# Performance work log

Hardware: AMD Instinct MI355X
Metric: run time of the kernel (lower is better)

The kernel has to match this reference:

```python
import jax, jax.numpy as jnp
import numpy as np

BETA_MAX = 0.995
BETA_MIN = 0.05
EPI_AGE_PENALTY = 0.02
EPI_STRENGTH_BOOST = 0.5
EPI_STRENGTH_DECAY = 0.995
EPI_WRITE_ALPHA = 0.5
EVICT_AGE_BOOST = 0.05
EVICT_STR_PENALTY = 0.5
SLOT_TEMP = 50.0
SWITCH_TAU = 0.5

B, H, K, U, OBS, SSUM, PROJ = 2048, 256, 32, 128, 128, 128, 128


def setup_inputs() -> dict:
    key = jax.random.key(0)
    ks = jax.random.split(key, 20)
    def gl(k, shape, fan_in):
        return jax.random.normal(k, shape, jnp.float32) / np.sqrt(fan_in).astype(np.float32)
    inp = {}
    inp['h_prev'] = jax.random.normal(ks[0], (B, H), jnp.float32)
    inp['keys'] = jax.random.normal(ks[1], (B, K, H), jnp.float32)
    inp['vals'] = jax.random.normal(ks[2], (B, K, H), jnp.float32)
    inp['age'] = jax.random.uniform(ks[3], (B, K), jnp.float32) * 100.0
    inp['strength'] = jax.random.uniform(ks[4], (B, K), jnp.float32)
    inp['obs'] = jax.random.normal(ks[5], (B, OBS), jnp.float32)
    inp['ssum'] = jax.random.normal(ks[6], (B, SSUM), jnp.float32)
    inp['u_int_prev'] = jax.random.normal(ks[7], (B, U), jnp.float32)
    inp['step_in_macro'] = jax.random.randint(ks[8], (B,), 0, 4, jnp.int32)
    # learned parameters
    inp['W_obs'] = gl(ks[9], (OBS, PROJ), OBS); inp['b_obs'] = jnp.zeros((PROJ,), jnp.float32)
    inp['W_ssum'] = gl(ks[10], (SSUM, PROJ), SSUM); inp['b_ssum'] = jnp.zeros((PROJ,), jnp.float32)
    XIN = 2 * PROJ
    inp['Wi'] = gl(ks[11], (XIN, 3 * H), XIN); inp['bi'] = jnp.zeros((3 * H,), jnp.float32)
    inp['Wh'] = gl(ks[12], (H, 3 * H), H); inp['bhn'] = jnp.zeros((H,), jnp.float32)
    inp['W_gate'] = gl(ks[13], (H, 1), H); inp['b_gate'] = jnp.zeros((1,), jnp.float32)
    inp['W_mean'] = gl(ks[14], (2 * H, U), 2 * H); inp['b_mean'] = jnp.zeros((U,), jnp.float32)
    inp['u_logstd'] = jnp.full((U,), -1.0, jnp.float32)
    inp['W_beta'] = gl(ks[15], (2 * H, 1), 2 * H); inp['b_beta'] = jnp.zeros((1,), jnp.float32)
    inp['W_sw'] = gl(ks[16], (2 * H, 1), 2 * H); inp['b_sw'] = jnp.zeros((1,), jnp.float32)
    return inp


def reference(h_prev, keys, vals, age, strength, obs, ssum, u_int_prev, step_in_macro,
              W_obs, b_obs, W_ssum, b_ssum, Wi, bi, Wh, bhn, W_gate, b_gate,
              W_mean, b_mean, u_logstd, W_beta, b_beta, W_sw, b_sw):
    Kslots = keys.shape[1]
    # input projections + GRU step (flax GRUCell: h' = (1-z)*n + z*h)
    xo = jnp.tanh(obs @ W_obs + b_obs)
    xs = jnp.tanh(ssum @ W_ssum + b_ssum)
    x_in = jnp.concatenate([xo, xs], axis=-1)
    gi = x_in @ Wi + bi
    gh = h_prev @ Wh
    ir, iz, inn = jnp.split(gi, 3, axis=-1)
    hr, hz, hn = jnp.split(gh, 3, axis=-1)
    r = jax.nn.sigmoid(ir + hr)
    z = jax.nn.sigmoid(iz + hz)
    n = jnp.tanh(inn + r * (hn + bhn))
    h_t = (1.0 - z) * n + z * h_prev
    # write gate
    w_str = jax.nn.sigmoid(h_t @ W_gate + b_gate)  # [B,1]
    # episodic slot memory: cosine-sim read
    qn = h_t / (jnp.linalg.norm(h_t, axis=-1, keepdims=True) + 1e-6)
    kn = keys / (jnp.linalg.norm(keys, axis=-1, keepdims=True) + 1e-6)
    sim_r = jnp.einsum('bkd,bd->bk', kn, qn)
    logits = sim_r + EPI_STRENGTH_BOOST * jnp.log(jnp.clip(strength, 1e-3, 1.0)) - EPI_AGE_PENALTY * age
    w_read = jax.nn.softmax(logits, axis=-1)
    read_out = jnp.einsum('bk,bkd->bd', w_read, vals)
    # write addressing (write_vec == query_vec == h_t so sim_w == sim_r)
    wk_n = qn
    sim_w = sim_r
    evict = EVICT_AGE_BOOST * jnp.log1p(age) - EVICT_STR_PENALTY * strength
    write_soft = jax.nn.softmax(sim_w * SLOT_TEMP + evict, axis=-1)
    write_hard = jax.nn.one_hot(jnp.argmax(write_soft, axis=-1), Kslots, dtype=jnp.float32)
    write_w = jax.lax.stop_gradient(write_hard - write_soft) + write_soft  # straight-through
    ws = jnp.clip(w_str, 0.0, 1.0)  # [B,1]
    eff_rate = write_w * ws * EPI_WRITE_ALPHA  # [B,K]
    rate = eff_rate[:, :, None]
    keys_new = (1.0 - rate) * keys + rate * wk_n[:, None, :]
    vals_new = (1.0 - rate) * vals + rate * h_t[:, None, :]
    age_new = (age + 1.0) * (1.0 - write_w)
    str_new = strength * EPI_STRENGTH_DECAY
    str_new = jnp.clip(str_new + write_w * ws * (1.0 - str_new), 0.0, 1.0)
    # heads
    ctx = jnp.concatenate([h_t, read_out], axis=-1)
    mean = ctx @ W_mean + b_mean
    beta = BETA_MIN + (BETA_MAX - BETA_MIN) * jax.nn.sigmoid((ctx @ W_beta + b_beta)[:, 0])
    sw_prob = jax.nn.sigmoid((ctx @ W_sw + b_sw)[:, 0])
    # deterministic path (rng=None): u_prop = mean, threshold switch
    u_prop = mean
    switch_f = jnp.where(sw_prob > SWITCH_TAU, 1.0, 0.0)
    is_boundary = jnp.where(step_in_macro == 0, 1.0, 0.0)
    switch_f = jnp.maximum(switch_f, is_boundary)
    sw_f = switch_f[:, None]
    beta_eff = beta[:, None] * (1.0 - sw_f)
    u_int = beta_eff * u_int_prev + (1.0 - beta_eff) * u_prop
    return (h_t, keys_new, vals_new, age_new, str_new, u_prop,
            switch_f.astype(jnp.int32), u_int, beta, sw_prob)
```

## Files before the change

kernel.cpp:

```cpp
#include <hip/hip_runtime.h>
#include <math.h>

#define Bdim 2048
#define Hdim 256
#define KS 32
#define Udim 128
#define OBSD 128
#define PROJD 128
#define H3 768

__device__ __forceinline__ float sigm(float x){ return 1.0f/(1.0f+__expf(-x)); }

typedef float __attribute__((ext_vector_type(4))) f32x4;

__device__ __forceinline__ float4 ntload4(const float* p){
    f32x4 v = __builtin_nontemporal_load((const f32x4*)p);
    return make_float4(v.x, v.y, v.z, v.w);
}
__device__ __forceinline__ void ntstore4(float* p, float4 q){
    f32x4 v = {q.x, q.y, q.z, q.w};
    __builtin_nontemporal_store(v, (f32x4*)p);
}

__global__ __launch_bounds__(256) void kA1(
    const float* __restrict__ obs, const float* __restrict__ ssum,
    const float* __restrict__ W_obs, const float* __restrict__ b_obs,
    const float* __restrict__ W_ssum, const float* __restrict__ b_ssum,
    float* __restrict__ xin)
{
    __shared__ float s_in[2][8][128];
    const int t = threadIdx.x;
    const int r0 = blockIdx.x * 8;

    {
        int r = t >> 5, c4 = (t & 31) << 2;
        float4 v = *(const float4*)(obs + (size_t)(r0+r)*OBSD + c4);
        s_in[0][r][c4+0]=v.x; s_in[0][r][c4+1]=v.y; s_in[0][r][c4+2]=v.z; s_in[0][r][c4+3]=v.w;
        v = *(const float4*)(ssum + (size_t)(r0+r)*OBSD + c4);
        s_in[1][r][c4+0]=v.x; s_in[1][r][c4+1]=v.y; s_in[1][r][c4+2]=v.z; s_in[1][r][c4+3]=v.w;
    }
    __syncthreads();

    const int col = t & 127;
    const int src = t >> 7;
    const float* Wp = src ? W_ssum : W_obs;
    const float bb = src ? b_ssum[col] : b_obs[col];

    float acc[8] = {0,0,0,0,0,0,0,0};
    for (int i=0;i<128;i++){
        float w = Wp[i*PROJD + col];
        #pragma unroll
        for (int r=0;r<8;r++) acc[r] = fmaf(s_in[src][r][i], w, acc[r]);
    }
    #pragma unroll
    for (int r=0;r<8;r++)
        xin[(size_t)(r0+r)*256 + t] = tanhf(acc[r] + bb);
}

__global__ __launch_bounds__(256) void kG2(
    const float* __restrict__ xin, const float* __restrict__ hp,
    const float* __restrict__ Wi, const float* __restrict__ Wh,
    float* __restrict__ g)
{
    __shared__ float Xt[2][16][68];
    __shared__ float Wt[2][16][64];

    const int t = threadIdx.x;
    const int bx = blockIdx.x >> 4;
    const int by = blockIdx.x & 15;
    const int r0 = bx * 64;
    const int c0 = by * 64;

    const int kbeg = (c0 >= 768) ? 256 : 0;
    const int kend = (c0 >= 512 && c0 < 768) ? 256 : 512;
    const int nck  = (kend - kbeg) >> 4;

    const int sr  = t >> 2;
    const int sk4 = (t & 3) << 2;
    const size_t xbase = (size_t)(r0 + sr) * 256 + sk4;
    const int wk  = t >> 4;
    const int wc4 = (t & 15) << 2;
    const int cW  = (c0 < 512) ? c0 : (c0 - 256);

    const int rowA = (t & 15) << 2;
    const int colA = (t >> 4) << 2;

    float acc[4][4] = {{0.f}};
    float4 xr, wr;

    {
        const int k0 = kbeg;
        const float* xs = (k0 < 256) ? (xin + xbase + k0) : (hp + xbase + (k0 - 256));
        xr = *(const float4*)xs;
        const int k = k0 + wk;
        const float* wsrc = (k < 256) ? (Wi + (size_t)k*H3 + c0 + wc4)
                                      : (Wh + (size_t)(k-256)*H3 + cW + wc4);
        wr = *(const float4*)wsrc;
    }
    Xt[0][sk4+0][sr] = xr.x; Xt[0][sk4+1][sr] = xr.y;
    Xt[0][sk4+2][sr] = xr.z; Xt[0][sk4+3][sr] = xr.w;
    *(float4*)&Wt[0][wk][wc4] = wr;
    __syncthreads();

    for (int ck = 0; ck < nck; ck++){
        const int cur = ck & 1;
        const bool more = (ck + 1 < nck);
        if (more){
            const int k0 = kbeg + ((ck + 1) << 4);
            const float* xs = (k0 < 256) ? (xin + xbase + k0) : (hp + xbase + (k0 - 256));
            xr = *(const float4*)xs;
            const int k = k0 + wk;
            const float* wsrc = (k < 256) ? (Wi + (size_t)k*H3 + c0 + wc4)
                                          : (Wh + (size_t)(k-256)*H3 + cW + wc4);
            wr = *(const float4*)wsrc;
        }
        #pragma unroll
        for (int kk = 0; kk < 16; kk++){
            float4 a4 = *(const float4*)&Xt[cur][kk][rowA];
            float4 b4 = *(const float4*)&Wt[cur][kk][colA];
            float av[4] = {a4.x, a4.y, a4.z, a4.w};
            float bv[4] = {b4.x, b4.y, b4.z, b4.w};
            #pragma unroll
            for (int i=0;i<4;i++)
                #pragma unroll
                for (int j=0;j<4;j++)
                    acc[i][j] = fmaf(av[i], bv[j], acc[i][j]);
        }
        if (more){
            const int nxt = cur ^ 1;
            Xt[nxt][sk4+0][sr] = xr.x; Xt[nxt][sk4+1][sr] = xr.y;
            Xt[nxt][sk4+2][sr] = xr.z; Xt[nxt][sk4+3][sr] = xr.w;
            *(float4*)&Wt[nxt][wk][wc4] = wr;
            __syncthreads();
        }
    }

    #pragma unroll
    for (int i=0;i<4;i++){
        float4 o = make_float4(acc[i][0], acc[i][1], acc[i][2], acc[i][3]);
        *(float4*)&g[(size_t)(r0 + rowA + i)*1024 + c0 + colA] = o;
    }
}

__global__ __launch_bounds__(256) void kA3(
    const float* __restrict__ g, const float* __restrict__ h_prev,
    const float* __restrict__ bi, const float* __restrict__ bhn,
    const float* __restrict__ W_gate, const float* __restrict__ b_gate,
    float* __restrict__ out_h, float* __restrict__ ws_qn, float* __restrict__ ws_wstr)
{
    __shared__ float redA[8][4], redB[8][4];
    __shared__ float s_inv[8];
    const int t = threadIdx.x;
    const int r0 = blockIdx.x * 8;

    const float bir = bi[t], biz = bi[t+256], bin_ = bi[t+512];
    const float bh = bhn[t];
    const float wg = W_gate[t];
    const int lane = t & 63, wid = t >> 6;

    float hv[8];
    #pragma unroll
    for (int r=0;r<8;r++){
        const size_t gb = (size_t)(r0+r)*1024;
        float gr = g[gb + t];
        float gz = g[gb + 256 + t];
        float gni = g[gb + 512 + t];
        float gnh = g[gb + 768 + t];
        float hp = h_prev[(size_t)(r0+r)*Hdim + t];
        float rr = sigm(gr + bir);
        float zz = sigm(gz + biz);
        float nn = tanhf(gni + bin_ + rr*(gnh + bh));
        hv[r] = (1.0f - zz)*nn + zz*hp;
    }

    #pragma unroll
    for (int r=0;r<8;r++){
        float a = hv[r]*hv[r];
        float b2 = hv[r]*wg;
        #pragma unroll
        for (int off=32; off>=1; off>>=1){
            a  += __shfl_down(a, off);
            b2 += __shfl_down(b2, off);
        }
        if (lane==0){ redA[r][wid]=a; redB[r][wid]=b2; }
    }
    __syncthreads();
    if (t < 8){
        float ss = redA[t][0]+redA[t][1]+redA[t][2]+redA[t][3];
        float gd = redB[t][0]+redB[t][1]+redB[t][2]+redB[t][3];
        s_inv[t] = 1.0f/(sqrtf(ss) + 1e-6f);
        ws_wstr[r0+t] = sigm(gd + b_gate[0]);
    }
    __syncthreads();
    #pragma unroll
    for (int r=0;r<8;r++){
        out_h[(size_t)(r0+r)*Hdim + t] = hv[r];
        ws_qn[(size_t)(r0+r)*Hdim + t] = hv[r]*s_inv[r];
    }
}

__global__ __launch_bounds__(256) void kBC(
    const float* __restrict__ keys, const float* __restrict__ vals,
    const float* __restrict__ age, const float* __restrict__ strength,
    const float* __restrict__ h_t, const float* __restrict__ ws_qn,
    const float* __restrict__ ws_wstr,
    const float* __restrict__ u_int_prev, const int* __restrict__ step_in_macro,
    const float* __restrict__ W_mean, const float* __restrict__ b_mean,
    const float* __restrict__ W_beta, const float* __restrict__ b_beta,
    const float* __restrict__ W_sw, const float* __restrict__ b_sw,
    float* __restrict__ keys_new, float* __restrict__ vals_new,
    float* __restrict__ age_new, float* __restrict__ str_new,
    float* __restrict__ out_uprop, float* __restrict__ out_switch,
    float* __restrict__ out_uint, float* __restrict__ out_beta, float* __restrict__ out_swp)
{
    __shared__ float s_sim[KS], s_wr[KS], s_rate[KS];
    __shared__ float4 s_ro[4][64];
    __shared__ float s_ctx[512];
    __shared__ float s_part[2][128];
    __shared__ float s_red[2][4];
    __shared__ float s_beff;

    const int b = blockIdx.x;
    const int t = threadIdx.x, lane = t & 63, wid = t >> 6;

    float ag = 0.f, st = 0.f, wstr = 0.f;
    if (t < KS){
        ag = age[b*KS+t];
        st = strength[b*KS+t];
        wstr = ws_wstr[b];
    }

    const float4 q4 = ((const float4*)(ws_qn + (size_t)b*Hdim))[lane];
    const float4 h4 = ((const float4*)(h_t  + (size_t)b*Hdim))[lane];

    const float* Kb = keys + (size_t)b*KS*Hdim;
    const float* Vb = vals + (size_t)b*KS*Hdim;
    float4 kreg[8], vreg[8];
    float v[16];
    #pragma unroll
    for (int s=0;s<8;s++){
        const int k = wid*8 + s;
        kreg[s] = ntload4(Kb + k*Hdim + lane*4);
        vreg[s] = ntload4(Vb + k*Hdim + lane*4);
        v[2*s]   = kreg[s].x*q4.x + kreg[s].y*q4.y + kreg[s].z*q4.z + kreg[s].w*q4.w;
        v[2*s+1] = kreg[s].x*kreg[s].x + kreg[s].y*kreg[s].y + kreg[s].z*kreg[s].z + kreg[s].w*kreg[s].w;
    }

    {
        const bool hb5 = (lane & 32) != 0;
        #pragma unroll
        for (int i=0;i<8;i++){
            float send = hb5 ? v[i] : v[i+8];
            float recv = __shfl_xor(send, 32);
            v[i] = (hb5 ? v[i+8] : v[i]) + recv;
        }
        const bool hb4 = (lane & 16) != 0;
        #pragma unroll
        for (int i=0;i<4;i++){
            float send = hb4 ? v[i] : v[i+4];
            float recv = __shfl_xor(send, 16);
            v[i] = (hb4 ? v[i+4] : v[i]) + recv;
        }
        const bool hb3 = (lane & 8) != 0;
        #pragma unroll
        for (int i=0;i<2;i++){
            float send = hb3 ? v[i] : v[i+2];
            float recv = __shfl_xor(send, 8);
            v[i] = (hb3 ? v[i+2] : v[i]) + recv;
        }
        const bool hb2 = (lane & 4) != 0;
        {
            float send = hb2 ? v[0] : v[1];
            float recv = __shfl_xor(send, 4);
            v[0] = (hb2 ? v[1] : v[0]) + recv;
        }
        float r0 = v[0];
        r0 += __shfl_xor(r0, 2);
        r0 += __shfl_xor(r0, 1);
        float other = __shfl_xor(r0, 4);
        if ((lane & 7) == 0){
            s_sim[wid*8 + (lane>>3)] = r0 / (sqrtf(other) + 1e-6f);
        }
    }
    __syncthreads();

    if (t < KS){
        float sim = s_sim[t];
        float cl = fminf(fmaxf(st, 0.001f), 1.0f);
        float logit = sim + 0.5f*logf(cl) - 0.02f*ag;
        float wl = 50.0f*sim + 0.05f*log1pf(ag) - 0.5f*st;

        float lmax = logit;
        #pragma unroll
        for (int off=16; off>=1; off>>=1)
            lmax = fmaxf(lmax, __shfl_xor(lmax, off));
        float e = __expf(logit - lmax);
        float es = e;
        #pragma unroll
        for (int off=16; off>=1; off>>=1)
            es += __shfl_xor(es, off);

        float wm = wl; int ki = t;
        #pragma unroll
        for (int off=16; off>=1; off>>=1){
            float ow = __shfl_xor(wm, off);
            int   ok = __shfl_xor(ki, off);
            if (ow > wm || (ow == wm && ok < ki)){ wm = ow; ki = ok; }
        }

        s_wr[t] = e / es;
        float hard = (t == ki) ? 1.0f : 0.0f;
        s_rate[t] = hard * 0.5f * wstr;
        age_new[b*KS+t] = (ag + 1.0f)*(1.0f - hard);
        float sd = st*0.995f;
        float sn = sd + hard*wstr*(1.0f - sd);
        str_new[b*KS+t] = fminf(fmaxf(sn,0.f),1.f);
    }
    __syncthreads();

    float4 ro = make_float4(0.f,0.f,0.f,0.f);
    float* KNb = keys_new + (size_t)b*KS*Hdim;
    float* VNb = vals_new + (size_t)b*KS*Hdim;
    #pragma unroll
    for (int s=0;s<8;s++){
        const int k = wid*8 + s;
        const float wr = s_wr[k];
        const float rate = s_rate[k];
        const float om = 1.0f - rate;
        ro.x = fmaf(wr, vreg[s].x, ro.x);
        ro.y = fmaf(wr, vreg[s].y, ro.y);
        ro.z = fmaf(wr, vreg[s].z, ro.z);
        ro.w = fmaf(wr, vreg[s].w, ro.w);
        float4 kn, vn;
        kn.x = om*kreg[s].x + rate*q4.x;
        kn.y = om*kreg[s].y + rate*q4.y;
        kn.z = om*kreg[s].z + rate*q4.z;
        kn.w = om*kreg[s].w + rate*q4.w;
        vn.x = om*vreg[s].x + rate*h4.x;
        vn.y = om*vreg[s].y + rate*h4.y;
        vn.z = om*vreg[s].z + rate*h4.z;
        vn.w = om*vreg[s].w + rate*h4.w;
        ntstore4(KNb + k*Hdim + lane*4, kn);
        ntstore4(VNb + k*Hdim + lane*4, vn);
    }
    s_ro[wid][lane] = ro;
    if (wid == 0){
        s_ctx[lane*4+0] = h4.x; s_ctx[lane*4+1] = h4.y;
        s_ctx[lane*4+2] = h4.z; s_ctx[lane*4+3] = h4.w;
    }
    __syncthreads();
    if (t < 64){
        float4 a = s_ro[0][t], bb = s_ro[1][t], c = s_ro[2][t], d = s_ro[3][t];
        s_ctx[256 + t*4+0] = a.x+bb.x+c.x+d.x;
        s_ctx[256 + t*4+1] = a.y+bb.y+c.y+d.y;
        s_ctx[256 + t*4+2] = a.z+bb.z+c.z+d.z;
        s_ctx[256 + t*4+3] = a.w+bb.w+c.w+d.w;
    }
    __syncthreads();

    {
        const int col = t & 127;
        const int kh  = t >> 7;
        const float* ctxh = s_ctx + kh*256;
        const float* Wm = W_mean + (size_t)kh*256*Udim + col;
        float acc = 0.f;
        #pragma unroll 4
        for (int i=0;i<256;i++)
            acc = fmaf(ctxh[i], Wm[(size_t)i*Udim], acc);
        s_part[kh][col] = acc;

        float cb = s_ctx[t]*W_beta[t] + s_ctx[t+256]*W_beta[t+256];
        float cs = s_ctx[t]*W_sw[t]   + s_ctx[t+256]*W_sw[t+256];
        #pragma unroll
        for (int off=32; off>=1; off>>=1){
            cb += __shfl_down(cb, off);
            cs += __shfl_down(cs, off);
        }
        if (lane == 0){ s_red[0][wid] = cb; s_red[1][wid] = cs; }
    }
    __syncthreads();
    if (t == 0){
        float db  = s_red[0][0]+s_red[0][1]+s_red[0][2]+s_red[0][3] + b_beta[0];
        float dsw = s_red[1][0]+s_red[1][1]+s_red[1][2]+s_red[1][3] + b_sw[0];
        float beta = 0.05f + 0.945f*sigm(db);
        float swp = sigm(dsw);
        float swf = (swp > 0.5f) ? 1.0f : 0.0f;
        if (step_in_macro[b] == 0) swf = 1.0f;
        out_beta[b]  = beta;
        out_swp[b]   = swp;
        out_switch[b]= swf;
        s_beff = beta*(1.0f - swf);
    }
    __syncthreads();
    if (t < 128){
        float mean = s_part[0][t] + s_part[1][t] + b_mean[t];
        size_t o = (size_t)b*Udim + t;
        out_uprop[o] = mean;
        float be = s_beff;
        out_uint[o] = be*u_int_prev[o] + (1.0f-be)*mean;
    }
}

extern "C" void kernel_launch(void* const* d_in, const int* in_sizes, int n_in,
                              void* d_out, int out_size, void* d_ws, size_t ws_size,
                              hipStream_t stream)
{
    const float* h_prev   = (const float*)d_in[0];
    const float* keys     = (const float*)d_in[1];
    const float* vals     = (const float*)d_in[2];
    const float* age      = (const float*)d_in[3];
    const float* strength = (const float*)d_in[4];
    const float* obs      = (const float*)d_in[5];
    const float* ssum     = (const float*)d_in[6];
    const float* u_int_prev = (const float*)d_in[7];
    const int*   step     = (const int*)d_in[8];
    const float* W_obs    = (const float*)d_in[9];
    const float* b_obs    = (const float*)d_in[10];
    const float* W_ssum   = (const float*)d_in[11];
    const float* b_ssum   = (const float*)d_in[12];
    const float* Wi       = (const float*)d_in[13];
    const float* bi       = (const float*)d_in[14];
    const float* Wh       = (const float*)d_in[15];
    const float* bhn      = (const float*)d_in[16];
    const float* W_gate   = (const float*)d_in[17];
    const float* b_gate   = (const float*)d_in[18];
    const float* W_mean   = (const float*)d_in[19];
    const float* b_mean   = (const float*)d_in[20];
    const float* W_beta   = (const float*)d_in[22];
    const float* b_beta   = (const float*)d_in[23];
    const float* W_sw     = (const float*)d_in[24];
    const float* b_sw     = (const float*)d_in[25];

    float* out = (float*)d_out;
    float* out_h    = out;
    float* out_kn   = out_h   + 524288;
    float* out_vn   = out_kn  + 16777216;
    float* out_age  = out_vn  + 16777216;
    float* out_str  = out_age + 65536;
    float* out_up   = out_str + 65536;
    float* out_sw   = out_up  + 262144;
    float* out_ui   = out_sw  + 2048;
    float* out_beta = out_ui  + 262144;
    float* out_swp  = out_beta+ 2048;

    float* ws = (float*)d_ws;
    float* ws_qn   = ws;
    float* ws_wstr = ws + Bdim*Hdim;

    float* ws_xin = out_vn;
    float* ws_g   = out_kn;

    kA1<<<Bdim/8, 256, 0, stream>>>(obs, ssum, W_obs, b_obs, W_ssum, b_ssum, ws_xin);
    kG2<<<512, 256, 0, stream>>>(ws_xin, h_prev, Wi, Wh, ws_g);
    kA3<<<Bdim/8, 256, 0, stream>>>(ws_g, h_prev, bi, bhn, W_gate, b_gate,
                                    out_h, ws_qn, ws_wstr);
    kBC<<<Bdim, 256, 0, stream>>>(keys, vals, age, strength, out_h, ws_qn, ws_wstr,
                                  u_int_prev, step, W_mean, b_mean,
                                  W_beta, b_beta, W_sw, b_sw,
                                  out_kn, out_vn, out_age, out_str,
                                  out_up, out_sw, out_ui, out_beta, out_swp);
}
```

Baseline: 125.9 us.

## Split head matmuls: compute h_t part in GRU kernel, read-out part in memory kernel

Moves the h_t half of the mean/beta/switch head projections from the per-row memory kernel into the GRU epilogue kernel, where 8 rows share each W_mean load, and leaves only the read-out half in kBC. It also stops writing the normalized query vector and stores only the inverse norm, which kBC applies to h_t on the fly. This is meant to cut W_mean traffic and the serial matmul work in the bandwidth-bound kBC, and to shrink workspace writes. The cost is extra workspace arrays and a larger kA3 with a 256-iteration matmul loop.

Measured after the change: 121.4 us. 3.5% less time.

```diff
diff --git a/kernel.cpp b/kernel.cpp
--- a/kernel.cpp
+++ b/kernel.cpp
@@ -146,16 +146,21 @@
     const float* __restrict__ g, const float* __restrict__ h_prev,
     const float* __restrict__ bi, const float* __restrict__ bhn,
     const float* __restrict__ W_gate, const float* __restrict__ b_gate,
-    float* __restrict__ out_h, float* __restrict__ ws_qn, float* __restrict__ ws_wstr)
+    const float* __restrict__ W_beta, const float* __restrict__ W_sw,
+    const float* __restrict__ W_mean,
+    float* __restrict__ out_h, float* __restrict__ ws_invn, float* __restrict__ ws_wstr,
+    float* __restrict__ ws_bh, float* __restrict__ ws_sh, float* __restrict__ ws_meanh)
 {
-    __shared__ float redA[8][4], redB[8][4];
-    __shared__ float s_inv[8];
+    __shared__ float s_h[8][256];
+    __shared__ float redA[8][4], redB[8][4], redC[8][4], redD[8][4];
     const int t = threadIdx.x;
     const int r0 = blockIdx.x * 8;
 
     const float bir = bi[t], biz = bi[t+256], bin_ = bi[t+512];
     const float bh = bhn[t];
     const float wg = W_gate[t];
+    const float wb = W_beta[t];
+    const float wsw = W_sw[t];
     const int lane = t & 63, wid = t >> 6;
 
     float hv[8];
@@ -171,39 +176,63 @@
         float zz = sigm(gz + biz);
         float nn = tanhf(gni + bin_ + rr*(gnh + bh));
         hv[r] = (1.0f - zz)*nn + zz*hp;
+        s_h[r][t] = hv[r];
     }
 
     #pragma unroll
     for (int r=0;r<8;r++){
         float a = hv[r]*hv[r];
         float b2 = hv[r]*wg;
+        float c2 = hv[r]*wb;
+        float d2 = hv[r]*wsw;
         #pragma unroll
         for (int off=32; off>=1; off>>=1){
             a  += __shfl_down(a, off);
             b2 += __shfl_down(b2, off);
-        }
-        if (lane==0){ redA[r][wid]=a; redB[r][wid]=b2; }
+            c2 += __shfl_down(c2, off);
+            d2 += __shfl_down(d2, off);
+        }
+        if (lane==0){ redA[r][wid]=a; redB[r][wid]=b2; redC[r][wid]=c2; redD[r][wid]=d2; }
     }
     __syncthreads();
     if (t < 8){
         float ss = redA[t][0]+redA[t][1]+redA[t][2]+redA[t][3];
         float gd = redB[t][0]+redB[t][1]+redB[t][2]+redB[t][3];
-        s_inv[t] = 1.0f/(sqrtf(ss) + 1e-6f);
+        float cb = redC[t][0]+redC[t][1]+redC[t][2]+redC[t][3];
+        float cs = redD[t][0]+redD[t][1]+redD[t][2]+redD[t][3];
+        ws_invn[r0+t] = 1.0f/(sqrtf(ss) + 1e-6f);
         ws_wstr[r0+t] = sigm(gd + b_gate[0]);
-    }
-    __syncthreads();
-    #pragma unroll
-    for (int r=0;r<8;r++){
+        ws_bh[r0+t] = cb;
+        ws_sh[r0+t] = cs;
+    }
+    #pragma unroll
+    for (int r=0;r<8;r++)
         out_h[(size_t)(r0+r)*Hdim + t] = hv[r];
-        ws_qn[(size_t)(r0+r)*Hdim + t] = hv[r]*s_inv[r];
+    __syncthreads();
+
+    {
+        const int col = t & 127;
+        const int rh = (t >> 7) * 4;
+        float acc[4] = {0,0,0,0};
+        #pragma unroll 8
+        for (int i=0;i<256;i++){
+            float w = W_mean[(size_t)i*Udim + col];
+            #pragma unroll
+            for (int j=0;j<4;j++) acc[j] = fmaf(s_h[rh+j][i], w, acc[j]);
+        }
+        #pragma unroll
+        for (int j=0;j<4;j++)
+            ws_meanh[(size_t)(r0+rh+j)*Udim + col] = acc[j];
     }
 }
 
 __global__ __launch_bounds__(256) void kBC(
     const float* __restrict__ keys, const float* __restrict__ vals,
     const float* __restrict__ age, const float* __restrict__ strength,
-    const float* __restrict__ h_t, const float* __restrict__ ws_qn,
-    const float* __restrict__ ws_wstr,
+    const float* __restrict__ h_t,
+    const float* __restrict__ ws_invn, const float* __restrict__ ws_wstr,
+    const float* __restrict__ ws_bh, const float* __restrict__ ws_sh,
+    const float* __restrict__ ws_meanh,
     const float* __restrict__ u_int_prev, const int* __restrict__ step_in_macro,
     const float* __restrict__ W_mean, const float* __restrict__ b_mean,
     const float* __restrict__ W_beta, const float* __restrict__ b_beta,
@@ -215,7 +244,7 @@
 {
     __shared__ float s_sim[KS], s_wr[KS], s_rate[KS];
     __shared__ float4 s_ro[4][64];
-    __shared__ float s_ctx[512];
+    __shared__ float s_rov[256];
     __shared__ float s_part[2][128];
     __shared__ float s_red[2][4];
     __shared__ float s_beff;
@@ -230,8 +259,9 @@
         wstr = ws_wstr[b];
     }
 
-    const float4 q4 = ((const float4*)(ws_qn + (size_t)b*Hdim))[lane];
-    const float4 h4 = ((const float4*)(h_t  + (size_t)b*Hdim))[lane];
+    const float invn = ws_invn[b];
+    const float4 h4 = ((const float4*)(h_t + (size_t)b*Hdim))[lane];
+    const float4 q4 = make_float4(h4.x*invn, h4.y*invn, h4.z*invn, h4.w*invn);
 
     const float* Kb = keys + (size_t)b*KS*Hdim;
     const float* Vb = vals + (size_t)b*KS*Hdim;
@@ -344,33 +374,29 @@
         ntstore4(VNb + k*Hdim + lane*4, vn);
     }
     s_ro[wid][lane] = ro;
-    if (wid == 0){
-        s_ctx[lane*4+0] = h4.x; s_ctx[lane*4+1] = h4.y;
-        s_ctx[lane*4+2] = h4.z; s_ctx[lane*4+3] = h4.w;
-    }
     __syncthreads();
     if (t < 64){
         float4 a = s_ro[0][t], bb = s_ro[1][t], c = s_ro[2][t], d = s_ro[3][t];
-        s_ctx[256 + t*4+0] = a.x+bb.x+c.x+d.x;
-        s_ctx[256 + t*4+1] = a.y+bb.y+c.y+d.y;
-        s_ctx[256 + t*4+2] = a.z+bb.z+c.z+d.z;
-        s_ctx[256 + t*4+3] = a.w+bb.w+c.w+d.w;
+        s_rov[t*4+0] = a.x+bb.x+c.x+d.x;
+        s_rov[t*4+1] = a.y+bb.y+c.y+d.y;
+        s_rov[t*4+2] = a.z+bb.z+c.z+d.z;
+        s_rov[t*4+3] = a.w+bb.w+c.w+d.w;
     }
     __syncthreads();
 
     {
         const int col = t & 127;
         const int kh  = t >> 7;
-        const float* ctxh = s_ctx + kh*256;
-        const float* Wm = W_mean + (size_t)kh*256*Udim + col;
+        const float* rop = s_rov + kh*128;
+        const float* Wm = W_mean + (size_t)(256 + kh*128)*Udim + col;
         float acc = 0.f;
-        #pragma unroll 4
-        for (int i=0;i<256;i++)
-            acc = fmaf(ctxh[i], Wm[(size_t)i*Udim], acc);
+        #pragma unroll 8
+        for (int i=0;i<128;i++)
+            acc = fmaf(rop[i], Wm[(size_t)i*Udim], acc);
         s_part[kh][col] = acc;
 
-        float cb = s_ctx[t]*W_beta[t] + s_ctx[t+256]*W_beta[t+256];
-        float cs = s_ctx[t]*W_sw[t]   + s_ctx[t+256]*W_sw[t+256];
+        float cb = s_rov[t]*W_beta[256+t];
+        float cs = s_rov[t]*W_sw[256+t];
         #pragma unroll
         for (int off=32; off>=1; off>>=1){
             cb += __shfl_down(cb, off);
@@ -380,8 +406,8 @@
     }
     __syncthreads();
     if (t == 0){
-        float db  = s_red[0][0]+s_red[0][1]+s_red[0][2]+s_red[0][3] + b_beta[0];
-        float dsw = s_red[1][0]+s_red[1][1]+s_red[1][2]+s_red[1][3] + b_sw[0];
+        float db  = s_red[0][0]+s_red[0][1]+s_red[0][2]+s_red[0][3] + ws_bh[b] + b_beta[0];
+        float dsw = s_red[1][0]+s_red[1][1]+s_red[1][2]+s_red[1][3] + ws_sh[b] + b_sw[0];
         float beta = 0.05f + 0.945f*sigm(db);
         float swp = sigm(dsw);
         float swf = (swp > 0.5f) ? 1.0f : 0.0f;
@@ -393,7 +419,7 @@
     }
     __syncthreads();
     if (t < 128){
-        float mean = s_part[0][t] + s_part[1][t] + b_mean[t];
+        float mean = ws_meanh[(size_t)b*Udim + t] + s_part[0][t] + s_part[1][t] + b_mean[t];
         size_t o = (size_t)b*Udim + t;
         out_uprop[o] = mean;
         float be = s_beff;
@@ -444,8 +470,11 @@
     float* out_swp  = out_beta+ 2048;
 
     float* ws = (float*)d_ws;
-    float* ws_qn   = ws;
-    float* ws_wstr = ws + Bdim*Hdim;
+    float* ws_invn  = ws;
+    float* ws_wstr  = ws + Bdim;
+    float* ws_bh    = ws + 2*Bdim;
+    float* ws_sh    = ws + 3*Bdim;
+    float* ws_meanh = ws + 4*Bdim;
 
     float* ws_xin = out_vn;
     float* ws_g   = out_kn;
@@ -453,8 +482,10 @@
     kA1<<<Bdim/8, 256, 0, stream>>>(obs, ssum, W_obs, b_obs, W_ssum, b_ssum, ws_xin);
     kG2<<<512, 256, 0, stream>>>(ws_xin, h_prev, Wi, Wh, ws_g);
     kA3<<<Bdim/8, 256, 0, stream>>>(ws_g, h_prev, bi, bhn, W_gate, b_gate,
-                                    out_h, ws_qn, ws_wstr);
-    kBC<<<Bdim, 256, 0, stream>>>(keys, vals, age, strength, out_h, ws_qn, ws_wstr,
+                                    W_beta, W_sw, W_mean,
+                                    out_h, ws_invn, ws_wstr, ws_bh, ws_sh, ws_meanh);
+    kBC<<<Bdim, 256, 0, stream>>>(keys, vals, age, strength, out_h,
+                                  ws_invn, ws_wstr, ws_bh, ws_sh, ws_meanh,
                                   u_int_prev, step, W_mean, b_mean,
                                   W_beta, b_beta, W_sw, b_sw,
                                   out_kn, out_vn, out_age, out_str,
```
